# Kernel optimization log

Hardware: AMD Instinct MI355X
Metric: run time of the kernel (lower is better)

The kernel has to match this reference:

```python
import jax, jax.numpy as jnp
import numpy as np

B, P, D = 64, 196, 768
HP = WP = 14
N_CLASSES = 200
C = N_CLASSES + 1
K_PROTO = 5
GAMMA = 0.999
TEMP = 0.2
EPS_SK = 0.05
SK_ITERS = 3


def l2norm(x, axis=-1, eps=1e-12):
    n = jnp.linalg.norm(x, axis=axis, keepdims=True)
    return x / jnp.maximum(n, eps)


def _safe_div(a, b):
    return a / jnp.where(b > 0, b, 1.0)


def masked_sinkhorn(L_cnk, mask):
    """Vectorized per-class Sinkhorn-Knopp over masked patch groups.
    L_cnk: [C, N, K] logits; mask: [C, N] bool (patch n belongs to class c).
    Returns Q: [C, K, N] (columns of each present class sum to 1)."""
    m = mask[:, None, :].astype(L_cnk.dtype)  # [C,1,N]
    Q = jnp.exp(jnp.transpose(L_cnk, (0, 2, 1)) / EPS_SK) * m  # [C,K,N]
    Q = _safe_div(Q, Q.sum(axis=(1, 2), keepdims=True))
    Nc = mask.sum(axis=1).astype(Q.dtype)[:, None, None]  # per-class patch count
    Nc_safe = jnp.where(Nc > 0, Nc, 1.0)
    for _ in range(SK_ITERS):
        Q = _safe_div(Q, Q.sum(axis=2, keepdims=True)) / K_PROTO  # row (prototype) norm
        Q = _safe_div(Q, Q.sum(axis=1, keepdims=True)) / Nc_safe  # col (patch) norm
    Q = Q * Nc  # undo final /Nc -> each patch column sums to 1
    return Q


def setup_inputs() -> dict:
    key = jax.random.key(0)
    k1, k2, k3, k4, k5 = jax.random.split(key, 5)
    patch_tokens = jax.random.normal(k1, (B, P, D), dtype=jnp.float32)
    raw_patch_tokens = jax.random.normal(k2, (B, P, D), dtype=jnp.float32)
    prototypes = 0.02 * jax.random.normal(k3, (C, K_PROTO, D), dtype=jnp.float32)
    sa_weights = jnp.full((N_CLASSES, K_PROTO), 0.5, dtype=jnp.float32)
    pseudo_patch_labels = jax.random.randint(k5, (B, HP, WP), 0, C, dtype=jnp.int32)
    return {
        "patch_tokens": patch_tokens,
        "raw_patch_tokens": raw_patch_tokens,
        "prototypes": prototypes,
        "sa_weights": sa_weights,
        "pseudo_patch_labels": pseudo_patch_labels,
    }


def reference(patch_tokens, raw_patch_tokens, prototypes, sa_weights, pseudo_patch_labels):
    # --- patch-prototype cosine similarity ---
    pt = l2norm(patch_tokens)                       # [B,P,D]
    proto_n = l2norm(prototypes)                    # [C,K,D]
    logits = jnp.einsum('bpd,ckd->bpck', pt, proto_n)  # [B,P,C,K]
    image_logits = logits.max(axis=1)               # [B,C,K]
    # --- ScoreAggregation classifier ---
    sw = jax.nn.softmax(sa_weights, axis=-1) * K_PROTO  # [n_classes,K]
    class_logits = (image_logits[:, :-1, :] * sw).sum(-1) / TEMP  # [B,n_classes]
    # --- online clustering (detached in original) ---
    rpt = l2norm(raw_patch_tokens)
    patches_flat = rpt.reshape(-1, D)               # [N,D], N=B*P
    labels_flat = pseudo_patch_labels.reshape(-1)   # [N]
    N = labels_flat.shape[0]
    L_nck = logits.reshape(N, C, K_PROTO)
    L_cnk = jnp.transpose(L_nck, (1, 0, 2))         # [C,N,K]
    mask = labels_flat[None, :] == jnp.arange(C)[:, None]  # [C,N]
    Q = masked_sinkhorn(L_cnk, mask)                # [C,K,N]
    # grouped GEMM: P_c_new = Q_c @ I_c for every class at once
    P_new_c = jnp.einsum('ckn,nd->ckd', Q, patches_flat)  # [C,K,D]
    present = mask.any(axis=1)[:, None, None]
    P_new = jnp.where(present,
                      GAMMA * prototypes + (1.0 - GAMMA) * P_new_c,
                      prototypes)
    # part assignment: argmax_k Q[label_n, k, n] + label_n * K
    Q_nck = jnp.transpose(Q, (2, 0, 1))             # [N,C,K]
    Q_at = Q_nck[jnp.arange(N), labels_flat]        # [N,K]
    assign = jnp.argmax(Q_at, axis=-1).astype(jnp.int32) + labels_flat * K_PROTO
    part_assignment_maps = assign.reshape(B, HP * WP)
    return (logits, image_logits, class_logits, part_assignment_maps, P_new)
```

## Files before the change

### kernel.cpp

```cpp
#include <hip/hip_runtime.h>
#include <math.h>

#define B_ 64
#define P_ 196
#define D_ 768
#define C_ 201
#define K_ 5
#define N_ (B_*P_)
#define CK_ (C_*K_)
#define NPAD 1024
#define NCLS 200
#define GAMMA_ 0.999f
#define INV_TEMP 5.0f
#define INV_EPS 20.0f
#define CAP2 256
#define MTILES 98
#define ROWS_TOT (2*N_ + NPAD)

typedef short s16x8 __attribute__((ext_vector_type(8)));
typedef float f32x4 __attribute__((ext_vector_type(4)));
typedef unsigned short u16x4 __attribute__((ext_vector_type(4)));

typedef __attribute__((address_space(3))) void lds_void;
typedef __attribute__((address_space(1))) const void g_void;
#define GLD16(gp, lp) __builtin_amdgcn_global_load_lds((g_void*)(gp), (lds_void*)(lp), 16, 0, 0)

__device__ __forceinline__ unsigned short f2bf(float f) {
    unsigned int u = __float_as_uint(f);
    unsigned int r = (u + 0x7FFFu + ((u >> 16) & 1u)) >> 16;
    return (unsigned short)r;
}

__global__ __launch_bounds__(256) void norm_all_kernel(
        const float* __restrict__ patch, const float* __restrict__ rawp,
        const float* __restrict__ proto, float* __restrict__ invR,
        unsigned short* __restrict__ Abf, unsigned short* __restrict__ Bbf,
        int* __restrict__ cnt) {
    if (blockIdx.x == 0 && threadIdx.x < C_) cnt[threadIdx.x] = 0;
    int gw = blockIdx.x * 4 + (threadIdx.x >> 6);
    int lane = threadIdx.x & 63;
    const float* src; unsigned short* dst; int realR; int r; bool wantInv = false;
    if (gw < N_) { r = gw; src = patch; dst = Abf; realR = N_; }
    else if (gw < 2 * N_) { r = gw - N_; src = rawp; dst = nullptr; realR = N_; wantInv = true; }
    else { r = gw - 2 * N_; src = proto; dst = Bbf; realR = CK_; }
    unsigned short* brow = dst ? dst + (size_t)r * D_ : nullptr;
    if (r >= realR) {
        u16x4 z = (u16x4)0;
        *(u16x4*)(brow + lane * 4)       = z;
        *(u16x4*)(brow + lane * 4 + 256) = z;
        *(u16x4*)(brow + lane * 4 + 512) = z;
        return;
    }
    const float4* row4 = (const float4*)(src + (size_t)r * D_);
    float4 v0 = row4[lane], v1 = row4[lane + 64], v2 = row4[lane + 128];
    float s = v0.x*v0.x + v0.y*v0.y + v0.z*v0.z + v0.w*v0.w
            + v1.x*v1.x + v1.y*v1.y + v1.z*v1.z + v1.w*v1.w
            + v2.x*v2.x + v2.y*v2.y + v2.z*v2.z + v2.w*v2.w;
#pragma unroll
    for (int o = 1; o < 64; o <<= 1) s += __shfl_xor(s, o, 64);
    float sc = 1.f / fmaxf(sqrtf(s), 1e-12f);
    if (brow) {
        u16x4 p0 = { f2bf(v0.x*sc), f2bf(v0.y*sc), f2bf(v0.z*sc), f2bf(v0.w*sc) };
        u16x4 p1 = { f2bf(v1.x*sc), f2bf(v1.y*sc), f2bf(v1.z*sc), f2bf(v1.w*sc) };
        u16x4 p2 = { f2bf(v2.x*sc), f2bf(v2.y*sc), f2bf(v2.z*sc), f2bf(v2.w*sc) };
        *(u16x4*)(brow + lane * 4)       = p0;
        *(u16x4*)(brow + lane * 4 + 256) = p1;
        *(u16x4*)(brow + lane * 4 + 512) = p2;
    } else if (wantInv && lane == 0) invR[r] = sc;
}

#define BM 128
#define BN 128
#define BKq 32
__global__ __launch_bounds__(256) void gemm_mfma_kernel(
    const unsigned short* __restrict__ Ab, const unsigned short* __restrict__ Bb,
    float* __restrict__ Cc,
    float* __restrict__ part) {
    __shared__ short As[BM * BKq];
    __shared__ short Bs[BN * BKq];
    __shared__ float maxw[4][2][BN];
    int tid = threadIdx.x;
    int mBase = blockIdx.y * BM;
    int nBase = blockIdx.x * BN;
    int w = tid >> 6;
    int lane = tid & 63;
    int wm = (w >> 1) * 64;
    int wn = (w & 1) * 64;
    int mrow = lane & 15;
    int kq = (lane >> 4) * 8;

    f32x4 acc[4][4];
#pragma unroll
    for (int i = 0; i < 4; ++i)
#pragma unroll
        for (int j = 0; j < 4; ++j) acc[i][j] = (f32x4)(0.f);

    int c0 = tid, c1 = tid + 256;
    const unsigned short* ga0 = Ab + (size_t)(mBase + (c0 >> 2)) * D_ + (c0 & 3) * 8;
    const unsigned short* ga1 = Ab + (size_t)(mBase + (c1 >> 2)) * D_ + (c1 & 3) * 8;
    const unsigned short* gb0 = Bb + (size_t)(nBase + (c0 >> 2)) * D_ + (c0 & 3) * 8;
    const unsigned short* gb1 = Bb + (size_t)(nBase + (c1 >> 2)) * D_ + (c1 & 3) * 8;
    short* la0 = As + c0 * 8;
    short* la1 = As + c1 * 8;
    short* lb0 = Bs + c0 * 8;
    short* lb1 = Bs + c1 * 8;

    for (int k0 = 0; k0 < D_; k0 += BKq) {
        GLD16(ga0 + k0, la0);
        GLD16(ga1 + k0, la1);
        GLD16(gb0 + k0, lb0);
        GLD16(gb1 + k0, lb1);
        __syncthreads();
        s16x8 a[4], b[4];
#pragma unroll
        for (int i = 0; i < 4; ++i)
            a[i] = *(const s16x8*)&As[(wm + 16 * i + mrow) * BKq + kq];
#pragma unroll
        for (int j = 0; j < 4; ++j)
            b[j] = *(const s16x8*)&Bs[(wn + 16 * j + mrow) * BKq + kq];
#pragma unroll
        for (int i = 0; i < 4; ++i)
#pragma unroll
            for (int j = 0; j < 4; ++j)
                acc[i][j] = __builtin_amdgcn_mfma_f32_16x16x32_bf16(a[i], b[j], acc[i][j], 0, 0, 0);
        __syncthreads();
    }

#pragma unroll
    for (int i = 0; i < 4; ++i) {
        int gm = mBase + wm + 16 * i + (lane >> 4) * 4;
#pragma unroll
        for (int j = 0; j < 4; ++j) {
            int gn = nBase + wn + 16 * j + (lane & 15);
            if (gn < CK_) {
                Cc[(size_t)(gm + 0) * CK_ + gn] = acc[i][j][0];
                Cc[(size_t)(gm + 1) * CK_ + gn] = acc[i][j][1];
                Cc[(size_t)(gm + 2) * CK_ + gn] = acc[i][j][2];
                Cc[(size_t)(gm + 3) * CK_ + gn] = acc[i][j][3];
            }
        }
    }

    int imgA = mBase / 196;
    int rstar = 196 * (imgA + 1);
#pragma unroll
    for (int j = 0; j < 4; ++j) {
        float m0 = -INFINITY, m1 = -INFINITY;
#pragma unroll
        for (int i = 0; i < 4; ++i) {
            int gm = mBase + wm + 16 * i + (lane >> 4) * 4;
#pragma unroll
            for (int r = 0; r < 4; ++r) {
                float v = acc[i][j][r];
                if (gm + r >= rstar) m1 = fmaxf(m1, v); else m0 = fmaxf(m0, v);
            }
        }
        m0 = fmaxf(m0, __shfl_xor(m0, 16)); m0 = fmaxf(m0, __shfl_xor(m0, 32));
        m1 = fmaxf(m1, __shfl_xor(m1, 16)); m1 = fmaxf(m1, __shfl_xor(m1, 32));
        if (lane < 16) {
            maxw[w][0][wn + 16 * j + lane] = m0;
            maxw[w][1][wn + 16 * j + lane] = m1;
        }
    }
    __syncthreads();
    int s = tid >> 7, col = tid & 127, h = col >> 6;
    float vmax = fmaxf(maxw[h][s][col], maxw[h + 2][s][col]);
    part[(size_t)(blockIdx.y * 2 + s) * 1024 + nBase + col] = vmax;
}

__global__ void imgcls_kernel(const float* __restrict__ part, const float* __restrict__ saw,
                              float* __restrict__ img, float* __restrict__ cls) {
    __shared__ float simg[CK_];
    int b = blockIdx.x;
    int t0 = (196 * b) >> 7;
    int t1 = (196 * b + 195) >> 7;
    for (int n = threadIdx.x; n < CK_; n += 256) {
        float m = -INFINITY;
        for (int t = t0; t <= t1; ++t) {
            int iA = (t << 7) / 196;
            int s = (iA == b) ? 0 : 1;
            m = fmaxf(m, part[(size_t)(t * 2 + s) * 1024 + n]);
        }
        img[b * CK_ + n] = m;
        simg[n] = m;
    }
    __syncthreads();
    int c = threadIdx.x;
    if (c < NCLS) {
        float w[K_];
        float mx = -INFINITY;
#pragma unroll
        for (int k = 0; k < K_; ++k) { w[k] = saw[c * K_ + k]; mx = fmaxf(mx, w[k]); }
        float ssum = 0.f;
#pragma unroll
        for (int k = 0; k < K_; ++k) { w[k] = expf(w[k] - mx); ssum += w[k]; }
        float acc = 0.f;
#pragma unroll
        for (int k = 0; k < K_; ++k)
            acc += simg[c * K_ + k] * (w[k] / ssum * (float)K_);
        cls[b * NCLS + c] = acc * INV_TEMP;
    }
}

__global__ void compact_kernel(const float* __restrict__ L, const int* __restrict__ labels,
                               int* __restrict__ cnt, int* __restrict__ idxList,
                               float* __restrict__ EList) {
    int n = blockIdx.x * 256 + threadIdx.x;
    if (n >= N_) return;
    int c = labels[n];
    int slot = atomicAdd(&cnt[c], 1);
    if (slot < CAP2) {
        idxList[c * CAP2 + slot] = n;
        const float* lp = L + (size_t)n * CK_ + c * K_;
#pragma unroll
        for (int k = 0; k < K_; ++k)
            EList[((size_t)(c * K_ + k)) * CAP2 + slot] = expf(lp[k] * INV_EPS);
    }
}

#define NJ (CAP2/64)
__global__ __launch_bounds__(256) void sinkhorn_kernel(
    const int* __restrict__ cnt, const int* __restrict__ idxList,
    const float* __restrict__ EList, const float* __restrict__ invR,
    float* __restrict__ WList, float* __restrict__ outAssign) {
    int c = blockIdx.x * 4 + (threadIdx.x >> 6);
    if (c >= C_) return;
    int lane = threadIdx.x & 63;
    int Nc = cnt[c]; if (Nc > CAP2) Nc = CAP2;
    if (Nc == 0) return;
    float e[NJ][K_];
    float cn[NJ];
    int idx[NJ];
#pragma unroll
    for (int j = 0; j < NJ; ++j) {
        int n = j * 64 + lane;
        bool v = n < Nc;
        cn[j] = v ? 1.f : 0.f;
        idx[j] = v ? idxList[c * CAP2 + n] : 0;
#pragma unroll
        for (int k = 0; k < K_; ++k)
            e[j][k] = v ? EList[((size_t)(c * K_ + k)) * CAP2 + n] : 0.f;
    }
    float r[K_];
    for (int it = 0; it < 3; ++it) {
#pragma unroll
        for (int k = 0; k < K_; ++k) {
            float s = 0.f;
#pragma unroll
            for (int j = 0; j < NJ; ++j) s += e[j][k] * cn[j];
            for (int o = 32; o > 0; o >>= 1) s += __shfl_xor(s, o, 64);
            r[k] = 1.f / ((float)K_ * s);
        }
#pragma unroll
        for (int j = 0; j < NJ; ++j) {
            float t = 0.f;
#pragma unroll
            for (int k = 0; k < K_; ++k) t += e[j][k] * r[k];
            cn[j] = (j * 64 + lane < Nc) ? 1.f / ((float)Nc * t) : 0.f;
        }
    }
#pragma unroll
    for (int j = 0; j < NJ; ++j) {
        int n = j * 64 + lane;
        if (n >= Nc) continue;
        int kb = 0; float best = e[j][0] * r[0];
#pragma unroll
        for (int k = 1; k < K_; ++k) {
            float v = e[j][k] * r[k];
            if (v > best) { best = v; kb = k; }
        }
        outAssign[idx[j]] = (float)(kb + c * K_);
        float scale = cn[j] * (float)Nc * (1.0f - GAMMA_) * invR[idx[j]];
#pragma unroll
        for (int k = 0; k < K_; ++k)
            WList[((size_t)(c * K_ + k)) * CAP2 + n] = e[j][k] * r[k] * scale;
    }
}

__global__ __launch_bounds__(192) void ema_kernel(
    const int* __restrict__ cnt, const int* __restrict__ idxList,
    const float* __restrict__ WList, const float* __restrict__ rawP,
    const float* __restrict__ proto, float* __restrict__ outProto) {
    int c = blockIdx.x;
    int d = blockIdx.y * 192 + threadIdx.x;
    int Nc = cnt[c]; if (Nc > CAP2) Nc = CAP2;
    size_t protoOff = (size_t)c * K_ * D_;
    if (Nc == 0) {
#pragma unroll
        for (int k = 0; k < K_; ++k)
            outProto[protoOff + (size_t)k * D_ + d] = proto[protoOff + (size_t)k * D_ + d];
        return;
    }
    __shared__ int s_idx[CAP2];
    __shared__ float s_w[K_][CAP2];
    for (int i = threadIdx.x; i < Nc; i += 192) {
        s_idx[i] = idxList[c * CAP2 + i];
#pragma unroll
        for (int k = 0; k < K_; ++k) s_w[k][i] = WList[((size_t)(c * K_ + k)) * CAP2 + i];
    }
    __syncthreads();
    float acc[K_] = {};
    int n = 0;
    for (; n + 1 < Nc; n += 2) {
        float v0 = rawP[(size_t)s_idx[n] * D_ + d];
        float v1 = rawP[(size_t)s_idx[n + 1] * D_ + d];
#pragma unroll
        for (int k = 0; k < K_; ++k) {
            acc[k] = fmaf(s_w[k][n], v0, acc[k]);
            acc[k] = fmaf(s_w[k][n + 1], v1, acc[k]);
        }
    }
    if (n < Nc) {
        float v0 = rawP[(size_t)s_idx[n] * D_ + d];
#pragma unroll
        for (int k = 0; k < K_; ++k) acc[k] = fmaf(s_w[k][n], v0, acc[k]);
    }
#pragma unroll
    for (int k = 0; k < K_; ++k)
        outProto[protoOff + (size_t)k * D_ + d] =
            fmaf(GAMMA_, proto[protoOff + (size_t)k * D_ + d], acc[k]);
}

extern "C" void kernel_launch(void* const* d_in, const int* in_sizes, int n_in,
                              void* d_out, int out_size, void* d_ws, size_t ws_size,
                              hipStream_t stream) {
    (void)in_sizes; (void)n_in; (void)out_size; (void)ws_size;
    const float* patch  = (const float*)d_in[0];
    const float* rawp   = (const float*)d_in[1];
    const float* proto  = (const float*)d_in[2];
    const float* saw    = (const float*)d_in[3];
    const int*   labels = (const int*)d_in[4];

    float* out    = (float*)d_out;
    float* logits = out;
    float* img    = out + 12606720;
    float* cls    = out + 12671040;
    float* assign = out + 12683840;
    float* pnew   = out + 12696384;

    float* ws   = (float*)d_ws;
    float* invR = ws;
    unsigned short* Abf = (unsigned short*)(ws + N_);
    unsigned short* Bbf = Abf + (size_t)N_ * D_;
    int*   cnt     = (int*)(Bbf + (size_t)NPAD * D_);
    int*   idxList = cnt + 256;
    float* EList   = (float*)(idxList + C_ * CAP2);
    float* WList   = EList + (size_t)C_ * K_ * CAP2;
    float* part    = WList + (size_t)C_ * K_ * CAP2;

    norm_all_kernel<<<ROWS_TOT / 4, 256, 0, stream>>>(patch, rawp, proto, invR, Abf, Bbf, cnt);
    gemm_mfma_kernel<<<dim3(NPAD / BN, MTILES), 256, 0, stream>>>(Abf, Bbf, logits, part);
    imgcls_kernel<<<B_, 256, 0, stream>>>(part, saw, img, cls);
    compact_kernel<<<(N_ + 255) / 256, 256, 0, stream>>>(logits, labels, cnt, idxList, EList);
    sinkhorn_kernel<<<(C_ + 3) / 4, 256, 0, stream>>>(cnt, idxList, EList, invR, WList, assign);
    ema_kernel<<<dim3(C_, 4), 192, 0, stream>>>(cnt, idxList, WList, rawp, proto, pnew);
}
```

Measured before the change: 208.3 us.

## Double-buffer LDS tiles in the MFMA GEMM and swizzle block-to-tile mapping

The GEMM mainloop now uses two LDS buffers per operand, so the async global-to-LDS load of the next K slice is issued before the MFMAs on the current slice run, and one barrier per iteration is dropped. Block IDs are also remapped so consecutive blocks share N tiles across M, which should improve L2 reuse on the XCD layout. The cost is twice the LDS for A/B, which may lower occupancy. There is also a risk that the async loads are not waited on correctly before the barrier.

```diff
diff --git a/kernel.cpp b/kernel.cpp
--- a/kernel.cpp
+++ b/kernel.cpp
@@ -76,12 +76,16 @@
     const unsigned short* __restrict__ Ab, const unsigned short* __restrict__ Bb,
     float* __restrict__ Cc,
     float* __restrict__ part) {
-    __shared__ short As[BM * BKq];
-    __shared__ short Bs[BN * BKq];
+    __shared__ short As[2][BM * BKq];
+    __shared__ short Bs[2][BN * BKq];
     __shared__ float maxw[4][2][BN];
     int tid = threadIdx.x;
-    int mBase = blockIdx.y * BM;
-    int nBase = blockIdx.x * BN;
+    int bid = blockIdx.y * 8 + blockIdx.x;
+    int swz = (bid & 7) * MTILES + (bid >> 3);
+    int mtile = swz >> 3;
+    int ntile = swz & 7;
+    int mBase = mtile * BM;
+    int nBase = ntile * BN;
     int w = tid >> 6;
     int lane = tid & 63;
     int wm = (w >> 1) * 64;
@@ -100,30 +104,34 @@
     const unsigned short* ga1 = Ab + (size_t)(mBase + (c1 >> 2)) * D_ + (c1 & 3) * 8;
     const unsigned short* gb0 = Bb + (size_t)(nBase + (c0 >> 2)) * D_ + (c0 & 3) * 8;
     const unsigned short* gb1 = Bb + (size_t)(nBase + (c1 >> 2)) * D_ + (c1 & 3) * 8;
-    short* la0 = As + c0 * 8;
-    short* la1 = As + c1 * 8;
-    short* lb0 = Bs + c0 * 8;
-    short* lb1 = Bs + c1 * 8;
-
+
+    auto stage = [&](int buf, int k0) {
+        GLD16(ga0 + k0, &As[buf][c0 * 8]);
+        GLD16(ga1 + k0, &As[buf][c1 * 8]);
+        GLD16(gb0 + k0, &Bs[buf][c0 * 8]);
+        GLD16(gb1 + k0, &Bs[buf][c1 * 8]);
+    };
+
+    stage(0, 0);
+    __syncthreads();
+    int cur = 0;
     for (int k0 = 0; k0 < D_; k0 += BKq) {
-        GLD16(ga0 + k0, la0);
-        GLD16(ga1 + k0, la1);
-        GLD16(gb0 + k0, lb0);
-        GLD16(gb1 + k0, lb1);
-        __syncthreads();
+        int nk = k0 + BKq;
+        if (nk < D_) stage(cur ^ 1, nk);
         s16x8 a[4], b[4];
 #pragma unroll
         for (int i = 0; i < 4; ++i)
-            a[i] = *(const s16x8*)&As[(wm + 16 * i + mrow) * BKq + kq];
+            a[i] = *(const s16x8*)&As[cur][(wm + 16 * i + mrow) * BKq + kq];
 #pragma unroll
         for (int j = 0; j < 4; ++j)
-            b[j] = *(const s16x8*)&Bs[(wn + 16 * j + mrow) * BKq + kq];
+            b[j] = *(const s16x8*)&Bs[cur][(wn + 16 * j + mrow) * BKq + kq];
 #pragma unroll
         for (int i = 0; i < 4; ++i)
 #pragma unroll
             for (int j = 0; j < 4; ++j)
                 acc[i][j] = __builtin_amdgcn_mfma_f32_16x16x32_bf16(a[i], b[j], acc[i][j], 0, 0, 0);
         __syncthreads();
+        cur ^= 1;
     }
 
 #pragma unroll
@@ -165,7 +173,7 @@
     __syncthreads();
     int s = tid >> 7, col = tid & 127, h = col >> 6;
     float vmax = fmaxf(maxw[h][s][col], maxw[h + 2][s][col]);
-    part[(size_t)(blockIdx.y * 2 + s) * 1024 + nBase + col] = vmax;
+    part[(size_t)(mtile * 2 + s) * 1024 + nBase + col] = vmax;
 }
 
 __global__ void imgcls_kernel(const float* __restrict__ part, const float* __restrict__ saw,
```

After: 202.2 us. 1.03x faster.
